# Optimization experiments

Measured on AMD Instinct MI355X. Metric: run time of the kernel, lower is better.

Reference implementation:

```python
import jax, jax.numpy as jnp
import numpy as np

D_MODEL = 768
N_HEADS = 12
D_HEAD = 64
N_MEM = 3072
ALPHA = 0.1
EPS = 1e-5
W_SCALE = 0.02  # standard init scale so energies/grads stay well-conditioned


def setup_inputs() -> dict:
    key = jax.random.key(0)
    k0, k1, k2, k3 = jax.random.split(key, 4)
    B, S = 8, 1024
    x = jax.random.normal(k0, (B, S, D_MODEL), jnp.float32)
    gamma = jnp.ones((1,), jnp.float32)                      # scalar LN gamma (ET uses a single gamma)
    delta = jnp.zeros((D_MODEL,), jnp.float32)               # LN bias
    Wq = jax.random.normal(k1, (N_HEADS, D_HEAD, D_MODEL), jnp.float32) * W_SCALE
    Wk = jax.random.normal(k2, (N_HEADS, D_HEAD, D_MODEL), jnp.float32) * W_SCALE
    beta = jnp.ones((N_HEADS,), jnp.float32) / np.sqrt(D_HEAD)  # per-head beta init 1/sqrt(d_head)
    xi = jax.random.normal(k3, (N_MEM, D_MODEL), jnp.float32) * W_SCALE
    return {"x": x, "gamma": gamma, "delta": delta, "Wq": Wq, "Wk": Wk,
            "beta": beta, "xi": xi, "n_steps": 12}


def _total_energy(x, gamma, delta, Wq, Wk, beta, xi):
    # --- EnergyLayerNorm: g = dL/dx, E_ln = <x, g> - L ---
    mean = jnp.mean(x, axis=-1, keepdims=True)
    xm = x - mean
    var = jnp.mean(xm * xm, axis=-1, keepdims=True)
    std = jnp.sqrt(var + EPS)
    g = gamma * xm / std + delta                       # (B,S,D)
    L = jnp.sum(D_MODEL * gamma * std) + jnp.sum(delta * x)
    e_ln = jnp.sum(x * g) - L
    # --- EnergyAttention: E = -sum_{b,h,q} (1/beta_h) * logsumexp_k(beta_h * Q.K) ---
    q = jnp.einsum('bsd,hyd->bhsy', g, Wq)
    k = jnp.einsum('bsd,hyd->bhsy', g, Wk)
    A = jnp.einsum('bhqy,bhky->bhqk', q, k)            # (B,H,S,S)
    lse = jax.nn.logsumexp(beta[None, :, None, None] * A, axis=-1)  # (B,H,S)
    e_attn = -jnp.sum(lse / beta[None, :, None])
    # --- HopfieldNetwork: E = -1/2 sum relu(g @ xi^T)^2 ---
    h = jnp.einsum('bsd,md->bsm', g, xi)               # (B,S,M)
    e_hop = -0.5 * jnp.sum(jnp.square(jax.nn.relu(h)))
    return e_ln + e_attn + e_hop


def reference(x, gamma, delta, Wq, Wk, beta, xi, n_steps):
    grad_fn = jax.grad(_total_energy, argnums=0)

    def step(state, _):
        return state - ALPHA * grad_fn(state, gamma, delta, Wq, Wk, beta, xi), None

    final, _ = jax.lax.scan(step, x, None, length=n_steps)
    return final
```

## Files before the change

### kernel.cpp

```cpp
#include <hip/hip_runtime.h>
#include <hip/hip_bf16.h>
#include <stdint.h>

#define T_TOK 8192
#define DM    768
#define NH    12
#define DH    64
#define SEQ   1024
#define NBH   96
#define NMEM  3072
#define NUP   4608
#define ALPHA 0.1f
#define EPS   1e-5f
#define NSTEPS 12
#define PAD   72
#define SPLITK 3

typedef unsigned short us;
typedef __bf16 bf16x8 __attribute__((ext_vector_type(8)));
typedef float  f32x4  __attribute__((ext_vector_type(4)));

__device__ __forceinline__ us f2bf(float f) {
  uint32_t u = __builtin_bit_cast(uint32_t, f);
  u += 0x7fffu + ((u >> 16) & 1u);
  return (us)(u >> 16);
}

__device__ __forceinline__ f32x4 mfma16(bf16x8 a, bf16x8 b, f32x4 c) {
  return __builtin_amdgcn_mfma_f32_16x16x32_bf16(a, b, c, 0, 0, 0);
}

__device__ __forceinline__ void gld16(const void* g, void* l) {
  __builtin_amdgcn_global_load_lds(
      (const __attribute__((address_space(1))) void*)(uintptr_t)g,
      (__attribute__((address_space(3))) void*)(uint32_t)(uintptr_t)l,
      16, 0, 0);
}

__device__ __forceinline__ float block_sum(float v, float* sb, int tid) {
#pragma unroll
  for (int d = 32; d >= 1; d >>= 1) v += __shfl_xor(v, d);
  __syncthreads();
  if ((tid & 63) == 0) sb[tid >> 6] = v;
  __syncthreads();
  return sb[0] + sb[1] + sb[2] + sb[3];
}

__global__ __launch_bounds__(256) void pack_w(const float* __restrict__ Wq,
                                              const float* __restrict__ Wk,
                                              const float* __restrict__ xi,
                                              us* __restrict__ Wup, us* __restrict__ WdT) {
  int idx = blockIdx.x * 256 + threadIdx.x;
  if (idx >= NUP * DM) return;
  int r = idx / DM, d = idx - r * DM;
  float v = (r < 768) ? Wq[idx] : (r < 1536 ? Wk[idx - 768 * DM] : xi[idx - 1536 * DM]);
  us h = f2bf(v);
  Wup[idx] = h;
  WdT[(size_t)d * NUP + r] = h;
}

__global__ __launch_bounds__(256) void ln_fwd(const float* __restrict__ X,
                                              const float* __restrict__ gamma,
                                              const float* __restrict__ delta,
                                              us* __restrict__ g_bf,
                                              float* __restrict__ meanb, float* __restrict__ rstdb) {
  int t = blockIdx.x, tid = threadIdx.x;
  const float* x = X + (size_t)t * DM;
  __shared__ float sb[4];
  float v0 = x[tid], v1 = x[tid + 256], v2 = x[tid + 512];
  float mean = block_sum(v0 + v1 + v2, sb, tid) * (1.0f / DM);
  float d0 = v0 - mean, d1 = v1 - mean, d2 = v2 - mean;
  float var = block_sum(d0 * d0 + d1 * d1 + d2 * d2, sb, tid) * (1.0f / DM);
  float rstd = rsqrtf(var + EPS);
  float gm = gamma[0];
  us* go = g_bf + (size_t)t * DM;
  go[tid]       = f2bf(gm * d0 * rstd + delta[tid]);
  go[tid + 256] = f2bf(gm * d1 * rstd + delta[tid + 256]);
  go[tid + 512] = f2bf(gm * d2 * rstd + delta[tid + 512]);
  if (tid == 0) { meanb[t] = mean; rstdb[t] = rstd; }
}

template <int MODE>
__global__ __launch_bounds__(512, 2) void gemm_bt(const us* __restrict__ A, const us* __restrict__ B,
                                                  int Kstride, int kchunk, us* __restrict__ QKout,
                                                  us* __restrict__ Dout, float* __restrict__ Gout) {
  __shared__ us As[3 * 256 * 32];
  __shared__ us Bs[3 * 256 * 32];
  int tid = threadIdx.x;
  int w = tid >> 6, lane = tid & 63, lm = lane & 15, lq = lane >> 4;
  int wm = w >> 2, wn = w & 3;

  int nwg  = gridDim.x * gridDim.y;
  int id   = blockIdx.y * gridDim.x + blockIdx.x;
  int qq   = nwg >> 3, rr = nwg & 7;
  int xcd  = id & 7, rank = id >> 3;
  int nid  = (xcd < rr ? xcd * (qq + 1) : rr * (qq + 1) + (xcd - rr) * qq) + rank;
  int bm   = nid % gridDim.x, bn = nid / gridDim.x;
  int m0 = bm * 256, n0 = bn * 256;
  int kbeg = blockIdx.z * kchunk;
  int NT = kchunk >> 5;

  int sr  = w * 16 + (lane >> 2);
  int k8s = (lane & 3) ^ ((lane >> 3) & 3);
  const us* pa = A + (size_t)(m0 + sr) * Kstride + kbeg + k8s * 8;
  const us* pb = B + (size_t)(n0 + sr) * Kstride + kbeg + k8s * 8;
  const size_t hstep = (size_t)128 * Kstride;
  us* dA0 = &As[tid * 8];
  us* dB0 = &Bs[tid * 8];

  int kx   = (lq ^ ((lm >> 1) & 3)) * 8;
  int aoff = (wm * 128 + lm) * 32 + kx;
  int boff = (wn * 64  + lm) * 32 + kx;
  const us* Ar = As + aoff;
  const us* Br = Bs + boff;

  f32x4 zero4 = {0.f, 0.f, 0.f, 0.f};
  f32x4 acc[8][4];
#pragma unroll
  for (int i = 0; i < 8; i++)
#pragma unroll
    for (int j = 0; j < 4; j++) acc[i][j] = zero4;

#define STAGE_A(S, T) { gld16(pa + (size_t)(T) * 32,         dA0 + (S) * 8192); \
                        gld16(pa + (size_t)(T) * 32 + hstep, dA0 + (S) * 8192 + 4096); }
#define STAGE_B(S, T) { gld16(pb + (size_t)(T) * 32,         dB0 + (S) * 8192); \
                        gld16(pb + (size_t)(T) * 32 + hstep, dB0 + (S) * 8192 + 4096); }

  STAGE_A(0, 0); STAGE_B(0, 0);
  STAGE_A(1, 1); STAGE_B(1, 1);
  asm volatile("s_waitcnt vmcnt(4)" ::: "memory");
  __builtin_amdgcn_s_barrier();

#define ITER(T, S) {                                                            \
    bf16x8 af_[4], bf_[4];                                                      \
    _Pragma("unroll") for (int x = 0; x < 4; x++)                               \
      af_[x] = *(const bf16x8*)(Ar + (S) * 8192 + x * 512);                     \
    _Pragma("unroll") for (int x = 0; x < 4; x++)                               \
      bf_[x] = *(const bf16x8*)(Br + (S) * 8192 + x * 512);                     \
    if ((T) + 2 < NT) STAGE_A(((S) + 2) % 3, (T) + 2);                          \
    __builtin_amdgcn_s_barrier();                                               \
    __builtin_amdgcn_s_setprio(1);                                              \
    _Pragma("unroll") for (int mt = 0; mt < 4; mt++)                            \
      _Pragma("unroll") for (int nt = 0; nt < 4; nt++)                          \
        acc[mt][nt] = mfma16(af_[mt], bf_[nt], acc[mt][nt]);                    \
    __builtin_amdgcn_s_setprio(0);                                              \
    __builtin_amdgcn_s_barrier();                                               \
    _Pragma("unroll") for (int x = 0; x < 4; x++)                               \
      af_[x] = *(const bf16x8*)(Ar + (S) * 8192 + (x + 4) * 512);               \
    if ((T) + 2 < NT) STAGE_B(((S) + 2) % 3, (T) + 2);                          \
    __builtin_amdgcn_s_barrier();                                               \
    __builtin_amdgcn_s_setprio(1);                                              \
    _Pragma("unroll") for (int mt = 0; mt < 4; mt++)                            \
      _Pragma("unroll") for (int nt = 0; nt < 4; nt++)                          \
        acc[mt + 4][nt] = mfma16(af_[mt], bf_[nt], acc[mt + 4][nt]);            \
    __builtin_amdgcn_s_setprio(0);                                              \
    asm volatile("s_waitcnt lgkmcnt(0)" ::: "memory");                          \
    if ((T) + 2 < NT)      { asm volatile("s_waitcnt vmcnt(4)" ::: "memory"); } \
    else if ((T) + 1 < NT) { asm volatile("s_waitcnt vmcnt(0)" ::: "memory"); } \
    __builtin_amdgcn_s_barrier();                                               \
  }

  for (int t = 0; t < NT; t += 3) {
    ITER(t,     0);
    ITER(t + 1, 1);
    ITER(t + 2, 2);
  }
#undef ITER
#undef STAGE_A
#undef STAGE_B

  float* Gz = (MODE == 1) ? Gout + (size_t)blockIdx.z * T_TOK * DM : nullptr;
#pragma unroll
  for (int mt = 0; mt < 8; mt++) {
    int row = m0 + wm * 128 + mt * 16 + lq * 4;
#pragma unroll
    for (int nt = 0; nt < 4; nt++) {
      int col = n0 + wn * 64 + nt * 16 + lm;
#pragma unroll
      for (int r = 0; r < 4; r++) {
        float v = acc[mt][nt][r];
        if (MODE == 0) {
          if (col < 1536) QKout[(size_t)(row + r) * 1536 + col] = f2bf(v);
          else            Dout[(size_t)(row + r) * NUP + col]   = f2bf(fmaxf(v, 0.f));
        } else {
          Gz[(size_t)(row + r) * DM + col] = v;
        }
      }
    }
  }
}

__global__ __launch_bounds__(256) void transpose_qk(const us* __restrict__ QK,
                                                    us* __restrict__ Qt, us* __restrict__ Kt) {
  int bh = blockIdx.x, kt = blockIdx.y, which = blockIdx.z;
  int b = bh / NH, h = bh - b * NH;
  int tid = threadIdx.x;
  __shared__ us tile[64][72];
  int c0 = h * 64 + (which ? 768 : 0);
  us* dst = (which ? Kt : Qt) + (size_t)bh * 64 * 1024;
#pragma unroll
  for (int r = 0; r < 2; r++) {
    int key = r * 32 + (tid >> 3); int yb = (tid & 7) * 8;
    *(bf16x8*)&tile[key][yb] =
        *(const bf16x8*)&QK[(size_t)(b * SEQ + kt * 64 + key) * 1536 + c0 + yb];
  }
  __syncthreads();
#pragma unroll
  for (int r = 0; r < 2; r++) {
    int lin = r * 256 + tid; int y = lin >> 3; int kb = (lin & 7) * 8;
    __align__(16) us tmp[8];
#pragma unroll
    for (int j = 0; j < 8; j++) tmp[j] = tile[kb + j][y];
    *(bf16x8*)&dst[(size_t)y * 1024 + kt * 64 + kb] = *(bf16x8*)tmp;
  }
}

__global__ __launch_bounds__(256) void attn_fwd(const us* __restrict__ QK, const us* __restrict__ Ktg,
                                                const float* __restrict__ beta,
                                                us* __restrict__ Dbuf, float* __restrict__ lse) {
  __shared__ us Qs[64 * PAD];
  __shared__ us Ks[64 * PAD];
  __shared__ us Kts[64 * PAD];
  __shared__ us Ps[4 * 16 * PAD];
  int bh = blockIdx.x, qt = blockIdx.y;
  int b = bh / NH, h = bh - b * NH;
  int tid = threadIdx.x, w = tid >> 6, lane = tid & 63, lm = lane & 15, lq = lane >> 4;
  float betah = beta[h];
#pragma unroll
  for (int r = 0; r < 2; r++) {
    int row = r * 32 + (tid >> 3); int yb = (tid & 7) * 8;
    *(bf16x8*)&Qs[row * PAD + yb] =
        *(const bf16x8*)&QK[(size_t)(b * SEQ + qt * 64 + row) * 1536 + h * 64 + yb];
  }
  __syncthreads();
  bf16x8 aq0 = *(const bf16x8*)&Qs[(w * 16 + lm) * PAD + lq * 8];
  bf16x8 aq1 = *(const bf16x8*)&Qs[(w * 16 + lm) * PAD + 32 + lq * 8];
  f32x4 zero = {0.f, 0.f, 0.f, 0.f};
  f32x4 O[4] = {zero, zero, zero, zero};
  float lacc[4] = {0.f, 0.f, 0.f, 0.f};
  us* pw = &Ps[w * 16 * PAD];

  for (int kc = 0; kc < SEQ; kc += 64) {
    __syncthreads();
#pragma unroll
    for (int r = 0; r < 2; r++) {
      int row = r * 32 + (tid >> 3); int yb = (tid & 7) * 8;
      *(bf16x8*)&Ks[row * PAD + yb] =
          *(const bf16x8*)&QK[(size_t)(b * SEQ + kc + row) * 1536 + 768 + h * 64 + yb];
      int lin = r * 256 + tid; int y = lin >> 3; int kb = (lin & 7) * 8;
      *(bf16x8*)&Kts[y * PAD + kb] =
          *(const bf16x8*)&Ktg[(size_t)(bh * 64 + y) * 1024 + kc + kb];
    }
    __syncthreads();
#pragma unroll
    for (int kk = 0; kk < 4; kk++) {
      f32x4 s = mfma16(aq0, *(const bf16x8*)&Ks[(kk * 16 + lm) * PAD + lq * 8], zero);
      s = mfma16(aq1, *(const bf16x8*)&Ks[(kk * 16 + lm) * PAD + 32 + lq * 8], s);
#pragma unroll
      for (int r = 0; r < 4; r++) {
        float p = __expf(betah * s[r]);
        lacc[r] += p;
        pw[(lq * 4 + r) * PAD + kk * 16 + lm] = f2bf(p);
      }
    }
    bf16x8 pa0 = *(const bf16x8*)&pw[lm * PAD + lq * 8];
    bf16x8 pa1 = *(const bf16x8*)&pw[lm * PAD + 32 + lq * 8];
#pragma unroll
    for (int nt = 0; nt < 4; nt++) {
      O[nt] = mfma16(pa0, *(const bf16x8*)&Kts[(nt * 16 + lm) * PAD + lq * 8], O[nt]);
      O[nt] = mfma16(pa1, *(const bf16x8*)&Kts[(nt * 16 + lm) * PAD + 32 + lq * 8], O[nt]);
    }
  }
  float l[4];
#pragma unroll
  for (int r = 0; r < 4; r++) {
    float v = lacc[r];
    v += __shfl_xor(v, 1); v += __shfl_xor(v, 2);
    v += __shfl_xor(v, 4); v += __shfl_xor(v, 8);
    l[r] = v;
  }
  float inv[4];
#pragma unroll
  for (int r = 0; r < 4; r++) inv[r] = 1.f / l[r];
#pragma unroll
  for (int nt = 0; nt < 4; nt++)
#pragma unroll
    for (int r = 0; r < 4; r++) {
      int q = qt * 64 + w * 16 + lq * 4 + r;
      Dbuf[(size_t)(b * SEQ + q) * NUP + h * 64 + nt * 16 + lm] = f2bf(O[nt][r] * inv[r]);
    }
  if (lm == 0) {
#pragma unroll
    for (int r = 0; r < 4; r++)
      lse[bh * SEQ + qt * 64 + w * 16 + lq * 4 + r] = __logf(l[r]);
  }
}

__global__ __launch_bounds__(256) void attn_bwd(const us* __restrict__ QK, const us* __restrict__ Qtg,
                                                const float* __restrict__ lse,
                                                const float* __restrict__ beta,
                                                us* __restrict__ Dbuf) {
  __shared__ us Ks2[64 * PAD];
  __shared__ us Qs2[64 * PAD];
  __shared__ us Qts[64 * PAD];
  __shared__ us Ps[4 * 16 * PAD];
  int bh = blockIdx.x, kt = blockIdx.y;
  int b = bh / NH, h = bh - b * NH;
  int tid = threadIdx.x, w = tid >> 6, lane = tid & 63, lm = lane & 15, lq = lane >> 4;
  float betah = beta[h];
#pragma unroll
  for (int r = 0; r < 2; r++) {
    int row = r * 32 + (tid >> 3); int yb = (tid & 7) * 8;
    *(bf16x8*)&Ks2[row * PAD + yb] =
        *(const bf16x8*)&QK[(size_t)(b * SEQ + kt * 64 + row) * 1536 + 768 + h * 64 + yb];
  }
  __syncthreads();
  bf16x8 ak0 = *(const bf16x8*)&Ks2[(w * 16 + lm) * PAD + lq * 8];
  bf16x8 ak1 = *(const bf16x8*)&Ks2[(w * 16 + lm) * PAD + 32 + lq * 8];
  f32x4 zero = {0.f, 0.f, 0.f, 0.f};
  f32x4 O[4] = {zero, zero, zero, zero};
  us* pw = &Ps[w * 16 * PAD];

  for (int qc = 0; qc < SEQ; qc += 64) {
    __syncthreads();
#pragma unroll
    for (int r = 0; r < 2; r++) {
      int row = r * 32 + (tid >> 3); int yb = (tid & 7) * 8;
      *(bf16x8*)&Qs2[row * PAD + yb] =
          *(const bf16x8*)&QK[(size_t)(b * SEQ + qc + row) * 1536 + h * 64 + yb];
      int lin = r * 256 + tid; int y = lin >> 3; int qb = (lin & 7) * 8;
      *(bf16x8*)&Qts[y * PAD + qb] =
          *(const bf16x8*)&Qtg[(size_t)(bh * 64 + y) * 1024 + qc + qb];
    }
    __syncthreads();
#pragma unroll
    for (int kk = 0; kk < 4; kk++) {
      f32x4 s = mfma16(ak0, *(const bf16x8*)&Qs2[(kk * 16 + lm) * PAD + lq * 8], zero);
      s = mfma16(ak1, *(const bf16x8*)&Qs2[(kk * 16 + lm) * PAD + 32 + lq * 8], s);
      float lv = lse[bh * SEQ + qc + kk * 16 + lm];
#pragma unroll
      for (int r = 0; r < 4; r++)
        pw[(lq * 4 + r) * PAD + kk * 16 + lm] = f2bf(__expf(betah * s[r] - lv));
    }
    bf16x8 pa0 = *(const bf16x8*)&pw[lm * PAD + lq * 8];
    bf16x8 pa1 = *(const bf16x8*)&pw[lm * PAD + 32 + lq * 8];
#pragma unroll
    for (int nt = 0; nt < 4; nt++) {
      O[nt] = mfma16(pa0, *(const bf16x8*)&Qts[(nt * 16 + lm) * PAD + lq * 8], O[nt]);
      O[nt] = mfma16(pa1, *(const bf16x8*)&Qts[(nt * 16 + lm) * PAD + 32 + lq * 8], O[nt]);
    }
  }
#pragma unroll
  for (int nt = 0; nt < 4; nt++)
#pragma unroll
    for (int r = 0; r < 4; r++) {
      int key = kt * 64 + w * 16 + lq * 4 + r;
      Dbuf[(size_t)(b * SEQ + key) * NUP + 768 + h * 64 + nt * 16 + lm] = f2bf(O[nt][r]);
    }
}

__global__ __launch_bounds__(256) void update_x(float* __restrict__ X, const float* __restrict__ G,
                                                float* __restrict__ meanb,
                                                float* __restrict__ rstdb,
                                                const float* __restrict__ gamma,
                                                const float* __restrict__ delta,
                                                us* __restrict__ g_bf) {
  int t = blockIdx.x, tid = threadIdx.x;
  __shared__ float sb[4];
  float mean = meanb[t], rstd = rstdb[t], gm = gamma[0];
  float* x = X + (size_t)t * DM;
  const float* g0 = G + (size_t)t * DM;
  const size_t GS = (size_t)T_TOK * DM;
  int i0 = tid, i1 = tid + 256, i2 = tid + 512;
  float x0 = x[i0], x1 = x[i1], x2 = x[i2];
  float gv0 = g0[i0] + g0[i0 + GS] + g0[i0 + 2 * GS];
  float gv1 = g0[i1] + g0[i1 + GS] + g0[i1 + 2 * GS];
  float gv2 = g0[i2] + g0[i2 + GS] + g0[i2 + 2 * GS];
  float v0 = x0 - gv0, v1 = x1 - gv1, v2 = x2 - gv2;
  float n0 = (x0 - mean) * rstd, n1 = (x1 - mean) * rstd, n2 = (x2 - mean) * rstd;
  float s1 = block_sum(v0 + v1 + v2, sb, tid) * (1.0f / DM);
  float s2 = block_sum(v0 * n0 + v1 * n1 + v2 * n2, sb, tid) * (1.0f / DM);
  float c = ALPHA * gm * rstd;
  float y0 = x0 - c * (v0 - s1 - n0 * s2);
  float y1 = x1 - c * (v1 - s1 - n1 * s2);
  float y2 = x2 - c * (v2 - s1 - n2 * s2);
  x[i0] = y0; x[i1] = y1; x[i2] = y2;
  float mean2 = block_sum(y0 + y1 + y2, sb, tid) * (1.0f / DM);
  float d0 = y0 - mean2, d1 = y1 - mean2, d2 = y2 - mean2;
  float var2 = block_sum(d0 * d0 + d1 * d1 + d2 * d2, sb, tid) * (1.0f / DM);
  float rstd2 = rsqrtf(var2 + EPS);
  us* go = g_bf + (size_t)t * DM;
  go[i0] = f2bf(gm * d0 * rstd2 + delta[i0]);
  go[i1] = f2bf(gm * d1 * rstd2 + delta[i1]);
  go[i2] = f2bf(gm * d2 * rstd2 + delta[i2]);
  if (tid == 0) { meanb[t] = mean2; rstdb[t] = rstd2; }
}

extern "C" void kernel_launch(void* const* d_in, const int* in_sizes, int n_in,
                              void* d_out, int out_size, void* d_ws, size_t ws_size,
                              hipStream_t stream) {
  const float* x_in  = (const float*)d_in[0];
  const float* gamma = (const float*)d_in[1];
  const float* delta = (const float*)d_in[2];
  const float* Wq    = (const float*)d_in[3];
  const float* Wk    = (const float*)d_in[4];
  const float* beta  = (const float*)d_in[5];
  const float* xi    = (const float*)d_in[6];
  float* X = (float*)d_out;

  char* p = (char*)d_ws;
  auto carve = [&](size_t bytes) -> char* {
    char* q = p; p += (bytes + 255) & ~(size_t)255; return q;
  };
  us*    g_bf  = (us*)carve((size_t)T_TOK * DM * 2);
  float* meanb = (float*)carve((size_t)T_TOK * 4);
  float* rstdb = (float*)carve((size_t)T_TOK * 4);
  us*    QK    = (us*)carve((size_t)T_TOK * 1536 * 2);
  us*    Qt    = (us*)carve((size_t)NBH * 64 * 1024 * 2);
  us*    Kt    = (us*)carve((size_t)NBH * 64 * 1024 * 2);
  float* lseb  = (float*)carve((size_t)NBH * SEQ * 4);
  us*    Dbuf  = (us*)carve((size_t)T_TOK * NUP * 2);
  float* G     = (float*)carve((size_t)SPLITK * T_TOK * DM * 4);
  us*    Wup   = (us*)carve((size_t)NUP * DM * 2);
  us*    WdT   = (us*)carve((size_t)DM * NUP * 2);

  hipMemcpyAsync(X, x_in, (size_t)T_TOK * DM * 4, hipMemcpyDeviceToDevice, stream);
  pack_w<<<(NUP * DM + 255) / 256, 256, 0, stream>>>(Wq, Wk, xi, Wup, WdT);
  ln_fwd<<<T_TOK, 256, 0, stream>>>(X, gamma, delta, g_bf, meanb, rstdb);

  for (int s = 0; s < NSTEPS; s++) {
    gemm_bt<0><<<dim3(32, 18, 1), 512, 0, stream>>>(g_bf, Wup, DM, DM, QK, Dbuf, nullptr);
    transpose_qk<<<dim3(NBH, 16, 2), 256, 0, stream>>>(QK, Qt, Kt);
    attn_fwd<<<dim3(NBH, 16), 256, 0, stream>>>(QK, Kt, beta, Dbuf, lseb);
    attn_bwd<<<dim3(NBH, 16), 256, 0, stream>>>(QK, Qt, lseb, beta, Dbuf);
    gemm_bt<1><<<dim3(32, 3, SPLITK), 512, 0, stream>>>(Dbuf, WdT, NUP, NUP / SPLITK,
                                                        nullptr, nullptr, G);
    update_x<<<T_TOK, 256, 0, stream>>>(X, G, meanb, rstdb, gamma, delta, g_bf);
  }
}
```

Measured before the change: 3.890 ms.

## Merge GEMM half-iterations into one MFMA burst, raise split-K, alias Qt/Kt into G

The GEMM inner iteration now loads all eight A fragments at once, issues both A and B prefetches together, and runs all 32 MFMAs in one block, dropping two barriers and the setprio toggles per k-step. Split-K for the down-projection goes from 3 to 4, giving more blocks and shorter K loops per block, and update_x sums the partials in a generic loop. The Qt/Kt scratch buffers now alias the G partial buffer, which is free while attention runs, cutting workspace and possibly cache footprint. The costs are higher register pressure from holding eight A fragments, less overlap between LDS reads and MFMAs, and one more partial buffer to write and read per step.

```diff
diff --git a/kernel.cpp b/kernel.cpp
--- a/kernel.cpp
+++ b/kernel.cpp
@@ -14,7 +14,7 @@
 #define EPS   1e-5f
 #define NSTEPS 12
 #define PAD   72
-#define SPLITK 3
+#define SPLITK 4
 
 typedef unsigned short us;
 typedef __bf16 bf16x8 __attribute__((ext_vector_type(8)));
@@ -132,28 +132,16 @@
   __builtin_amdgcn_s_barrier();
 
 #define ITER(T, S) {                                                            \
-    bf16x8 af_[4], bf_[4];                                                      \
-    _Pragma("unroll") for (int x = 0; x < 4; x++)                               \
+    bf16x8 af_[8], bf_[4];                                                      \
+    _Pragma("unroll") for (int x = 0; x < 8; x++)                               \
       af_[x] = *(const bf16x8*)(Ar + (S) * 8192 + x * 512);                     \
     _Pragma("unroll") for (int x = 0; x < 4; x++)                               \
       bf_[x] = *(const bf16x8*)(Br + (S) * 8192 + x * 512);                     \
-    if ((T) + 2 < NT) STAGE_A(((S) + 2) % 3, (T) + 2);                          \
-    __builtin_amdgcn_s_barrier();                                               \
-    __builtin_amdgcn_s_setprio(1);                                              \
-    _Pragma("unroll") for (int mt = 0; mt < 4; mt++)                            \
+    if ((T) + 2 < NT) { STAGE_A(((S) + 2) % 3, (T) + 2);                        \
+                        STAGE_B(((S) + 2) % 3, (T) + 2); }                      \
+    _Pragma("unroll") for (int mt = 0; mt < 8; mt++)                            \
       _Pragma("unroll") for (int nt = 0; nt < 4; nt++)                          \
         acc[mt][nt] = mfma16(af_[mt], bf_[nt], acc[mt][nt]);                    \
-    __builtin_amdgcn_s_setprio(0);                                              \
-    __builtin_amdgcn_s_barrier();                                               \
-    _Pragma("unroll") for (int x = 0; x < 4; x++)                               \
-      af_[x] = *(const bf16x8*)(Ar + (S) * 8192 + (x + 4) * 512);               \
-    if ((T) + 2 < NT) STAGE_B(((S) + 2) % 3, (T) + 2);                          \
-    __builtin_amdgcn_s_barrier();                                               \
-    __builtin_amdgcn_s_setprio(1);                                              \
-    _Pragma("unroll") for (int mt = 0; mt < 4; mt++)                            \
-      _Pragma("unroll") for (int nt = 0; nt < 4; nt++)                          \
-        acc[mt + 4][nt] = mfma16(af_[mt], bf_[nt], acc[mt + 4][nt]);            \
-    __builtin_amdgcn_s_setprio(0);                                              \
     asm volatile("s_waitcnt lgkmcnt(0)" ::: "memory");                          \
     if ((T) + 2 < NT)      { asm volatile("s_waitcnt vmcnt(4)" ::: "memory"); } \
     else if ((T) + 1 < NT) { asm volatile("s_waitcnt vmcnt(0)" ::: "memory"); } \
@@ -373,9 +361,13 @@
   const size_t GS = (size_t)T_TOK * DM;
   int i0 = tid, i1 = tid + 256, i2 = tid + 512;
   float x0 = x[i0], x1 = x[i1], x2 = x[i2];
-  float gv0 = g0[i0] + g0[i0 + GS] + g0[i0 + 2 * GS];
-  float gv1 = g0[i1] + g0[i1 + GS] + g0[i1 + 2 * GS];
-  float gv2 = g0[i2] + g0[i2 + GS] + g0[i2 + 2 * GS];
+  float gv0 = 0.f, gv1 = 0.f, gv2 = 0.f;
+#pragma unroll
+  for (int z = 0; z < SPLITK; z++) {
+    gv0 += g0[i0 + z * GS];
+    gv1 += g0[i1 + z * GS];
+    gv2 += g0[i2 + z * GS];
+  }
   float v0 = x0 - gv0, v1 = x1 - gv1, v2 = x2 - gv2;
   float n0 = (x0 - mean) * rstd, n1 = (x1 - mean) * rstd, n2 = (x2 - mean) * rstd;
   float s1 = block_sum(v0 + v1 + v2, sb, tid) * (1.0f / DM);
@@ -416,11 +408,11 @@
   float* meanb = (float*)carve((size_t)T_TOK * 4);
   float* rstdb = (float*)carve((size_t)T_TOK * 4);
   us*    QK    = (us*)carve((size_t)T_TOK * 1536 * 2);
-  us*    Qt    = (us*)carve((size_t)NBH * 64 * 1024 * 2);
-  us*    Kt    = (us*)carve((size_t)NBH * 64 * 1024 * 2);
+  float* G     = (float*)carve((size_t)SPLITK * T_TOK * DM * 4);
+  us*    Qt    = (us*)G;
+  us*    Kt    = Qt + (size_t)NBH * 64 * 1024;
   float* lseb  = (float*)carve((size_t)NBH * SEQ * 4);
   us*    Dbuf  = (us*)carve((size_t)T_TOK * NUP * 2);
-  float* G     = (float*)carve((size_t)SPLITK * T_TOK * DM * 4);
   us*    Wup   = (us*)carve((size_t)NUP * DM * 2);
   us*    WdT   = (us*)carve((size_t)DM * NUP * 2);
 
```

New measurement: 3.479 ms. 1.12x faster.
